# Kernel optimization log

Measured on AMD Instinct MI355X. Metric: run time of the kernel, lower is better.

Reference implementation:

```python
import jax, jax.numpy as jnp
import numpy as np

SOS = 28          # RNNTParam.SOS = num_labels - 1
NUM_EMBED = 28    # num_labels - 1
C = 320           # pred_hidden_size
L = 2             # pred_num_layers
U, N = 128, 512   # decode steps, batch


def setup_inputs() -> dict:
    key = jax.random.key(0)
    ks = jax.random.split(key, 8)
    s = 1.0 / np.sqrt(C).astype(np.float32)
    x = jax.random.randint(ks[0], (U, N), 0, 29)                       # labels incl. SOS=28
    h0 = jax.random.normal(ks[1], (L, N, C), jnp.float32)
    c0 = jax.random.normal(ks[2], (L, N, C), jnp.float32)
    embed_weight = jax.random.normal(ks[3], (NUM_EMBED, C), jnp.float32)
    w_ih = jax.random.uniform(ks[4], (L, 4 * C, C), jnp.float32, -s, s)
    w_hh = jax.random.uniform(ks[5], (L, 4 * C, C), jnp.float32, -s, s)
    b_ih = jax.random.uniform(ks[6], (L, 4 * C), jnp.float32, -s, s)
    b_hh = jax.random.uniform(ks[7], (L, 4 * C), jnp.float32, -s, s)
    return dict(x=x, h0=h0, c0=c0, embed_weight=embed_weight,
                w_ih=w_ih, w_hh=w_hh, b_ih=b_ih, b_hh=b_hh)


def _lstm_layer(xs, h0, c0, w_ih, w_hh, b_ih, b_hh):
    # xs: [U, N, C]; torch LSTM gate order: i, f, g, o
    bias = b_ih + b_hh                                   # [4C]
    gx = jnp.einsum('unc,gc->ung', xs, w_ih) + bias      # precompute input part

    def step(carry, gx_t):
        h, c = carry
        gates = gx_t + h @ w_hh.T                        # [N, 4C]
        i, f, g, o = jnp.split(gates, 4, axis=-1)
        i = jax.nn.sigmoid(i)
        f = jax.nn.sigmoid(f)
        g = jnp.tanh(g)
        o = jax.nn.sigmoid(o)
        c = f * c + i * g
        h = o * jnp.tanh(c)
        return (h, c), h

    (hT, cT), ys = jax.lax.scan(step, (h0, c0), gx)
    return ys, hT, cT


def reference(x, h0, c0, embed_weight, w_ih, w_hh, b_ih, b_hh):
    sos_mask = (x == SOS)                                # [U, N]
    idx = jnp.where(sos_mask, 0, x)
    g = embed_weight[idx]                                # [U, N, C]
    g = jnp.where(sos_mask[..., None], 0.0, g)

    hs, cs = [], []
    for layer in range(L):
        g, hT, cT = _lstm_layer(g, h0[layer], c0[layer],
                                w_ih[layer], w_hh[layer],
                                b_ih[layer], b_hh[layer])
        hs.append(hT)
        cs.append(cT)
    hg = jnp.stack(hs, axis=0)                           # [L, N, C]
    cg = jnp.stack(cs, axis=0)
    return g, (hg, cg)
```

## Files before the change

kernel.cpp:

```cpp
#include <hip/hip_runtime.h>
#include <hip/hip_bf16.h>
#include <stdint.h>


typedef short short8 __attribute__((ext_vector_type(8)));
typedef float f32x4 __attribute__((ext_vector_type(4)));

#define USTEPS 128
#define HSZ    (512*320)
#define GSTEP  (512*320)
#define HGOFF  (128*512*320)
#define CGOFF  (HGOFF + 2*512*320)
#define FLAGSTRIDE 16

__device__ __forceinline__ uint16_t f2bf(float f) {
  union { float f; uint32_t i; } v; v.f = f;
  uint32_t i = v.i;
  return (uint16_t)((i + 0x7fffu + ((i >> 16) & 1u)) >> 16);
}
__device__ __forceinline__ float rcp_(float x) { return __builtin_amdgcn_rcpf(x); }
__device__ __forceinline__ float sigm(float x) { return rcp_(1.0f + __expf(-x)); }
__device__ __forceinline__ float tanh_(float x) {
  float ax = fabsf(x);
  float e  = __expf(-2.0f * ax);
  float t  = (1.0f - e) * rcp_(1.0f + e);
  return x < 0.0f ? -t : t;
}
__device__ __forceinline__ uint4 cvt8(const float* s) {
  float4 a = ((const float4*)s)[0];
  float4 b = ((const float4*)s)[1];
  uint4 r;
  r.x = (uint32_t)f2bf(a.x) | ((uint32_t)f2bf(a.y) << 16);
  r.y = (uint32_t)f2bf(a.z) | ((uint32_t)f2bf(a.w) << 16);
  r.z = (uint32_t)f2bf(b.x) | ((uint32_t)f2bf(b.y) << 16);
  r.w = (uint32_t)f2bf(b.z) | ((uint32_t)f2bf(b.w) << 16);
  return r;
}
__device__ __forceinline__ short8 loadw8(const float* p) {
  float4 a = ((const float4*)p)[0];
  float4 b = ((const float4*)p)[1];
  short8 r;
  r[0] = (short)f2bf(a.x); r[1] = (short)f2bf(a.y);
  r[2] = (short)f2bf(a.z); r[3] = (short)f2bf(a.w);
  r[4] = (short)f2bf(b.x); r[5] = (short)f2bf(b.y);
  r[6] = (short)f2bf(b.z); r[7] = (short)f2bf(b.w);
  return r;
}

#define PREP_G0   (29 * 1280)
#define PREP_B1   (PREP_G0 + 1280)
#define PREP_FL   (PREP_B1 + 4096)
#define PREP_HI   (PREP_FL + 2 * 512 * 40)
__global__ void prep_kernel(const float* __restrict__ embed,
                            const float* __restrict__ w_ih,
                            const float* __restrict__ b_ih,
                            const float* __restrict__ b_hh,
                            const float* __restrict__ h0,
                            float* __restrict__ G0p,
                            float* __restrict__ bias1p,
                            uint32_t* __restrict__ flags,
                            uint16_t* __restrict__ Hx0,
                            uint16_t* __restrict__ Hx1) {
  int tid = blockIdx.x * blockDim.x + threadIdx.x;
  if (tid < PREP_G0) {
    int v = tid / 1280, col = tid % 1280;
    int hg = col / 80, idx = col % 80;
    int k = idx >> 2, q = idx & 3;
    int r = q * 320 + hg * 20 + k;
    float acc = b_ih[r] + b_hh[r];
    if (v < 28) {
      const float4* e = (const float4*)(embed + (size_t)v * 320);
      const float4* w = (const float4*)(w_ih + (size_t)r * 320);
#pragma unroll 4
      for (int i = 0; i < 80; ++i) {
        float4 a = e[i], b = w[i];
        acc += a.x * b.x + a.y * b.y + a.z * b.z + a.w * b.w;
      }
    }
    G0p[tid] = acc;
  } else if (tid < PREP_B1) {
    int col = tid - PREP_G0;
    int hg = col / 80, idx = col % 80;
    int k = idx >> 2, q = idx & 3;
    int r = q * 320 + hg * 20 + k;
    bias1p[col] = b_ih[1280 + r] + b_hh[1280 + r];
  } else if (tid < PREP_FL) {
    flags[tid - PREP_B1] = 0;
  } else if (tid < PREP_HI) {
    int id = tid - PREP_FL;
    int layer = id / 20480;
    int rem = id - layer * 20480;
    int n = rem / 40, c = rem - n * 40;
    const float* src = h0 + (size_t)layer * HSZ + (size_t)n * 320 + c * 8;
    uint16_t* dst = (layer ? Hx1 : Hx0) + HSZ + (size_t)n * 320 + c * 8;
    *(uint4*)dst = cvt8(src);
  }
}

__global__ void __launch_bounds__(320, 2)
rnnt_kernel(const int* __restrict__ x,
            const float* __restrict__ c0,
            const float* __restrict__ w_ih,
            const float* __restrict__ w_hh,
            const float* __restrict__ G0p,
            const float* __restrict__ bias1p,
            uint16_t* __restrict__ Hx0,
            uint16_t* __restrict__ Hx1,
            uint32_t* __restrict__ flags,
            float* __restrict__ out) {
  __shared__ __align__(16) uint16_t Hl0[32 * 320];
  __shared__ __align__(16) uint16_t Hl1[32 * 320];
  __shared__ __align__(16) float    gates0[32 * 84];
  __shared__ __align__(16) float    gates1[32 * 84];

  const int tid  = threadIdx.x;
  const int wave = tid >> 6;
  const int lane = tid & 63;
  const int quad = lane >> 4;
  const int lm   = lane & 15;
  const int blk  = blockIdx.x;
  const int bg = (blk & 7) * 2 + (blk >> 7);
  const int hg = (blk >> 3) & 15;

  short8 Bhh0[10], Bih1[10], Bhh1[10];
  {
    int ncol = wave * 16 + lm;
    int k = ncol >> 2, q = ncol & 3;
    int r = q * 320 + hg * 20 + k;
    const float* p0 = w_hh + (size_t)r * 320 + quad * 8;
    const float* p1 = w_hh + (size_t)(1280 + r) * 320 + quad * 8;
    const float* pi = w_ih + (size_t)(1280 + r) * 320 + quad * 8;
#pragma unroll
    for (int kk = 0; kk < 10; ++kk) {
      Bhh0[kk] = loadw8(p0 + kk * 32);
      Bhh1[kk] = loadw8(p1 + kk * 32);
      Bih1[kk] = loadw8(pi + kk * 32);
    }
  }
  const float bias1v = bias1p[hg * 80 + wave * 16 + lm];

  const int un  = tid / 10;
  const int ukp = tid - un * 10;
  const int n_g = bg * 32 + un;
  const int kc  = hg * 20 + ukp * 2;

  int smc[8], spc[8];
#pragma unroll
  for (int it = 0; it < 8; ++it) {
    int cid = tid + it * 320;
    int m = cid / 80;
    int c8 = cid - m * 80;
    int c16 = c8 >> 1, h = c8 & 1;
    int p16 = c16 + m; if (p16 >= 40) p16 -= 40;
    smc[it] = m * 320 + c8 * 4;
    spc[it] = m * 320 + p16 * 8 + h * 4;
  }
  const size_t gbase = (size_t)bg * 32 * 320;

  float c0s0 = c0[(size_t)n_g * 320 + kc];
  float c0s1 = c0[(size_t)n_g * 320 + kc + 1];
  float c1s0 = c0[(size_t)(512 + n_g) * 320 + kc];
  float c1s1 = c0[(size_t)(512 + n_g) * 320 + kc + 1];

  uint32_t* myflag = flags + (size_t)(bg * 16 + hg) * FLAGSTRIDE;

  float4 gxa, gxb;
  {
    const int v = x[n_g];
    const float* gx = G0p + (size_t)v * 1280 + hg * 80 + ukp * 8;
    gxa = ((const float4*)gx)[0];
    gxb = ((const float4*)gx)[1];
  }

#pragma unroll 1
  for (int t = 0; t <= USTEPS; ++t) {
    const bool do0 = (t < USTEPS);
    const bool do1 = (t >= 1);

    const uint16_t* s0b = Hx0 + (size_t)((t - 1) & 1) * HSZ + gbase;
    const uint16_t* s1b = Hx1 + (size_t)(t & 1) * HSZ + gbase;

    unsigned long long r0[8], r1[8];
#pragma unroll
    for (int it = 0; it < 8; ++it)
      r0[it] = __hip_atomic_load((unsigned long long*)(s0b + smc[it]),
                                 __ATOMIC_RELAXED, __HIP_MEMORY_SCOPE_AGENT);
#pragma unroll
    for (int it = 0; it < 8; ++it)
      r1[it] = __hip_atomic_load((unsigned long long*)(s1b + smc[it]),
                                 __ATOMIC_RELAXED, __HIP_MEMORY_SCOPE_AGENT);
#pragma unroll
    for (int it = 0; it < 8; ++it) {
      *(unsigned long long*)(Hl0 + spc[it]) = r0[it];
      *(unsigned long long*)(Hl1 + spc[it]) = r1[it];
    }
    __syncthreads();

    f32x4 ag00 = {0.f, 0.f, 0.f, 0.f}, ag01 = {0.f, 0.f, 0.f, 0.f};
    f32x4 ag10 = {bias1v, bias1v, bias1v, bias1v}, ag11 = ag10;
#pragma unroll
    for (int kk = 0; kk < 10; ++kk) {
      int cch = kk * 4 + quad;
      int p0a = cch + lm;      if (p0a >= 40) p0a -= 40;
      int p1a = cch + lm + 16; if (p1a >= 40) p1a -= 40;
      short8 a00 = *(const short8*)(Hl0 + lm * 320 + p0a * 8);
      short8 a01 = *(const short8*)(Hl0 + (lm + 16) * 320 + p1a * 8);
      if (do0) {
        ag00 = __builtin_amdgcn_mfma_f32_16x16x32_bf16(a00, Bhh0[kk], ag00, 0, 0, 0);
        ag01 = __builtin_amdgcn_mfma_f32_16x16x32_bf16(a01, Bhh0[kk], ag01, 0, 0, 0);
      }
      if (do1) {
        short8 a10 = *(const short8*)(Hl1 + lm * 320 + p0a * 8);
        short8 a11 = *(const short8*)(Hl1 + (lm + 16) * 320 + p1a * 8);
        ag10 = __builtin_amdgcn_mfma_f32_16x16x32_bf16(a00, Bih1[kk], ag10, 0, 0, 0);
        ag11 = __builtin_amdgcn_mfma_f32_16x16x32_bf16(a01, Bih1[kk], ag11, 0, 0, 0);
        ag10 = __builtin_amdgcn_mfma_f32_16x16x32_bf16(a10, Bhh1[kk], ag10, 0, 0, 0);
        ag11 = __builtin_amdgcn_mfma_f32_16x16x32_bf16(a11, Bhh1[kk], ag11, 0, 0, 0);
      }
    }

    if (do0) {
#pragma unroll
      for (int r = 0; r < 4; ++r) {
        gates0[(quad * 4 + r) * 84 + wave * 16 + lm]      = ag00[r];
        gates0[(16 + quad * 4 + r) * 84 + wave * 16 + lm] = ag01[r];
      }
    }
    if (do1) {
#pragma unroll
      for (int r = 0; r < 4; ++r) {
        gates1[(quad * 4 + r) * 84 + wave * 16 + lm]      = ag10[r];
        gates1[(16 + quad * 4 + r) * 84 + wave * 16 + lm] = ag11[r];
      }
    }
    __syncthreads();

    if (do0) {
      const float* gp = gates0 + un * 84 + ukp * 8;
      float i0 = gp[0] + gxa.x, f0 = gp[1] + gxa.y, g0 = gp[2] + gxa.z, o0 = gp[3] + gxa.w;
      float i1 = gp[4] + gxb.x, f1 = gp[5] + gxb.y, g1 = gp[6] + gxb.z, o1 = gp[7] + gxb.w;
      c0s0 = sigm(f0) * c0s0 + sigm(i0) * tanh_(g0);
      c0s1 = sigm(f1) * c0s1 + sigm(i1) * tanh_(g1);
      float ha = sigm(o0) * tanh_(c0s0);
      float hb = sigm(o1) * tanh_(c0s1);
      uint32_t packed = (uint32_t)f2bf(ha) | ((uint32_t)f2bf(hb) << 16);
      __hip_atomic_store((uint32_t*)(Hx0 + (size_t)(t & 1) * HSZ + (size_t)n_g * 320 + kc),
                         packed, __ATOMIC_RELAXED, __HIP_MEMORY_SCOPE_AGENT);
      if (t == USTEPS - 1) {
        *(float2*)(out + HGOFF + (size_t)n_g * 320 + kc) = make_float2(ha, hb);
        *(float2*)(out + CGOFF + (size_t)n_g * 320 + kc) = make_float2(c0s0, c0s1);
      }
    }

    if (do1) {
      const int u1 = t - 1;
      const float* gp = gates1 + un * 84 + ukp * 8;
      float i0 = gp[0], f0 = gp[1], g0 = gp[2], o0 = gp[3];
      float i1 = gp[4], f1 = gp[5], g1 = gp[6], o1 = gp[7];
      c1s0 = sigm(f0) * c1s0 + sigm(i0) * tanh_(g0);
      c1s1 = sigm(f1) * c1s1 + sigm(i1) * tanh_(g1);
      float ha = sigm(o0) * tanh_(c1s0);
      float hb = sigm(o1) * tanh_(c1s1);
      *(float2*)(out + (size_t)u1 * GSTEP + (size_t)n_g * 320 + kc) = make_float2(ha, hb);
      uint32_t packed = (uint32_t)f2bf(ha) | ((uint32_t)f2bf(hb) << 16);
      __hip_atomic_store((uint32_t*)(Hx1 + (size_t)((t + 1) & 1) * HSZ + (size_t)n_g * 320 + kc),
                         packed, __ATOMIC_RELAXED, __HIP_MEMORY_SCOPE_AGENT);
      if (t == USTEPS) {
        *(float2*)(out + HGOFF + (size_t)(512 + n_g) * 320 + kc) = make_float2(ha, hb);
        *(float2*)(out + CGOFF + (size_t)(512 + n_g) * 320 + kc) = make_float2(c1s0, c1s1);
      }
    }

    if (t + 1 < USTEPS) {
      const int v = x[(t + 1) * 512 + n_g];
      const float* gx = G0p + (size_t)v * 1280 + hg * 80 + ukp * 8;
      gxa = ((const float4*)gx)[0];
      gxb = ((const float4*)gx)[1];
    }

    if (t < USTEPS) {
      asm volatile("s_waitcnt vmcnt(0)" ::: "memory");
      __syncthreads();
      if (tid < 16) {
        if (tid == 0) {
          __hip_atomic_store(myflag, (uint32_t)(t + 1), __ATOMIC_RELAXED,
                             __HIP_MEMORY_SCOPE_AGENT);
        }
        uint32_t* peer = flags + (size_t)(bg * 16 + tid) * FLAGSTRIDE;
        while (__hip_atomic_load(peer, __ATOMIC_RELAXED,
                                 __HIP_MEMORY_SCOPE_AGENT) < (uint32_t)(t + 1)) {
        }
      }
      __syncthreads();
    }
  }
}

extern "C" void kernel_launch(void* const* d_in, const int* in_sizes, int n_in,
                              void* d_out, int out_size, void* d_ws, size_t ws_size,
                              hipStream_t stream) {
  (void)in_sizes; (void)n_in; (void)out_size; (void)ws_size;
  const int*   x     = (const int*)d_in[0];
  const float* h0    = (const float*)d_in[1];
  const float* c0    = (const float*)d_in[2];
  const float* embed = (const float*)d_in[3];
  const float* w_ih  = (const float*)d_in[4];
  const float* w_hh  = (const float*)d_in[5];
  const float* b_ih  = (const float*)d_in[6];
  const float* b_hh  = (const float*)d_in[7];
  float* out = (float*)d_out;

  char* ws = (char*)d_ws;
  float*    G0p   = (float*)(ws);
  float*    b1p   = (float*)(ws + 148480);
  uint32_t* flags = (uint32_t*)(ws + 153600);
  uint16_t* Hx0   = (uint16_t*)(ws + 169984);
  uint16_t* Hx1   = (uint16_t*)(ws + 825344);

  hipLaunchKernelGGL(prep_kernel, dim3(326), dim3(256), 0, stream,
                     embed, w_ih, b_ih, b_hh, h0, G0p, b1p, flags, Hx0, Hx1);

  void* args[] = { (void*)&x, (void*)&c0, (void*)&w_ih, (void*)&w_hh,
                   (void*)&G0p, (void*)&b1p, (void*)&Hx0, (void*)&Hx1,
                   (void*)&flags, (void*)&out };
  hipLaunchCooperativeKernel((const void*)rnnt_kernel, dim3(256), dim3(320),
                             args, 0, stream);
}
```

Baseline: 748.1 us.

## Split grid barrier into per-layer flags and overlap layer-1 loads with compute

```diff
diff --git a/kernel.cpp b/kernel.cpp
--- a/kernel.cpp
+++ b/kernel.cpp
@@ -49,7 +49,7 @@
 
 #define PREP_G0   (29 * 1280)
 #define PREP_B1   (PREP_G0 + 1280)
-#define PREP_FL   (PREP_B1 + 4096)
+#define PREP_FL   (PREP_B1 + 8192)
 #define PREP_HI   (PREP_FL + 2 * 512 * 40)
 __global__ void prep_kernel(const float* __restrict__ embed,
                             const float* __restrict__ w_ih,
@@ -112,6 +112,7 @@
   __shared__ __align__(16) uint16_t Hl1[32 * 320];
   __shared__ __align__(16) float    gates0[32 * 84];
   __shared__ __align__(16) float    gates1[32 * 84];
+  __shared__ int ctr0, ctr1;
 
   const int tid  = threadIdx.x;
   const int wave = tid >> 6;
@@ -162,7 +163,25 @@
   float c1s0 = c0[(size_t)(512 + n_g) * 320 + kc];
   float c1s1 = c0[(size_t)(512 + n_g) * 320 + kc + 1];
 
-  uint32_t* myflag = flags + (size_t)(bg * 16 + hg) * FLAGSTRIDE;
+  uint32_t* flags0  = flags;
+  uint32_t* flags1  = flags + 256 * FLAGSTRIDE;
+  uint32_t* myflag0 = flags0 + (size_t)(bg * 16 + hg) * FLAGSTRIDE;
+  uint32_t* myflag1 = flags1 + (size_t)(bg * 16 + hg) * FLAGSTRIDE;
+
+  {
+    if (tid == 0) { ctr0 = 0; ctr1 = 0; }
+    const uint16_t* s0b = Hx0 + HSZ + gbase;
+    unsigned long long r0[8];
+#pragma unroll
+    for (int it = 0; it < 8; ++it)
+      r0[it] = __hip_atomic_load((const unsigned long long*)(s0b + smc[it]),
+                                 __ATOMIC_RELAXED, __HIP_MEMORY_SCOPE_AGENT);
+    asm volatile("s_waitcnt vmcnt(0)" ::: "memory");
+#pragma unroll
+    for (int it = 0; it < 8; ++it)
+      *(unsigned long long*)(Hl0 + spc[it]) = r0[it];
+    __syncthreads();
+  }
 
   float4 gxa, gxb;
   {
@@ -177,24 +196,14 @@
     const bool do0 = (t < USTEPS);
     const bool do1 = (t >= 1);
 
-    const uint16_t* s0b = Hx0 + (size_t)((t - 1) & 1) * HSZ + gbase;
-    const uint16_t* s1b = Hx1 + (size_t)(t & 1) * HSZ + gbase;
-
-    unsigned long long r0[8], r1[8];
-#pragma unroll
-    for (int it = 0; it < 8; ++it)
-      r0[it] = __hip_atomic_load((unsigned long long*)(s0b + smc[it]),
-                                 __ATOMIC_RELAXED, __HIP_MEMORY_SCOPE_AGENT);
-#pragma unroll
-    for (int it = 0; it < 8; ++it)
-      r1[it] = __hip_atomic_load((unsigned long long*)(s1b + smc[it]),
-                                 __ATOMIC_RELAXED, __HIP_MEMORY_SCOPE_AGENT);
-#pragma unroll
-    for (int it = 0; it < 8; ++it) {
-      *(unsigned long long*)(Hl0 + spc[it]) = r0[it];
-      *(unsigned long long*)(Hl1 + spc[it]) = r1[it];
-    }
-    __syncthreads();
+    unsigned long long r1[8];
+    if (do1) {
+      const uint16_t* s1b = Hx1 + (size_t)(t & 1) * HSZ + gbase;
+#pragma unroll
+      for (int it = 0; it < 8; ++it)
+        r1[it] = __hip_atomic_load((const unsigned long long*)(s1b + smc[it]),
+                                   __ATOMIC_RELAXED, __HIP_MEMORY_SCOPE_AGENT);
+    }
 
     f32x4 ag00 = {0.f, 0.f, 0.f, 0.f}, ag01 = {0.f, 0.f, 0.f, 0.f};
     f32x4 ag10 = {bias1v, bias1v, bias1v, bias1v}, ag11 = ag10;
@@ -210,27 +219,22 @@
         ag01 = __builtin_amdgcn_mfma_f32_16x16x32_bf16(a01, Bhh0[kk], ag01, 0, 0, 0);
       }
       if (do1) {
-        short8 a10 = *(const short8*)(Hl1 + lm * 320 + p0a * 8);
-        short8 a11 = *(const short8*)(Hl1 + (lm + 16) * 320 + p1a * 8);
         ag10 = __builtin_amdgcn_mfma_f32_16x16x32_bf16(a00, Bih1[kk], ag10, 0, 0, 0);
         ag11 = __builtin_amdgcn_mfma_f32_16x16x32_bf16(a01, Bih1[kk], ag11, 0, 0, 0);
-        ag10 = __builtin_amdgcn_mfma_f32_16x16x32_bf16(a10, Bhh1[kk], ag10, 0, 0, 0);
-        ag11 = __builtin_amdgcn_mfma_f32_16x16x32_bf16(a11, Bhh1[kk], ag11, 0, 0, 0);
-      }
-    }
-
+      }
+    }
+
+    if (do1) {
+      asm volatile("s_waitcnt vmcnt(0)" ::: "memory");
+#pragma unroll
+      for (int it = 0; it < 8; ++it)
+        *(unsigned long long*)(Hl1 + spc[it]) = r1[it];
+    }
     if (do0) {
 #pragma unroll
       for (int r = 0; r < 4; ++r) {
         gates0[(quad * 4 + r) * 84 + wave * 16 + lm]      = ag00[r];
         gates0[(16 + quad * 4 + r) * 84 + wave * 16 + lm] = ag01[r];
-      }
-    }
-    if (do1) {
-#pragma unroll
-      for (int r = 0; r < 4; ++r) {
-        gates1[(quad * 4 + r) * 84 + wave * 16 + lm]      = ag10[r];
-        gates1[(16 + quad * 4 + r) * 84 + wave * 16 + lm] = ag11[r];
       }
     }
     __syncthreads();
@@ -251,6 +255,48 @@
         *(float2*)(out + CGOFF + (size_t)n_g * 320 + kc) = make_float2(c0s0, c0s1);
       }
     }
+
+    if (do1) {
+#pragma unroll
+      for (int kk = 0; kk < 5; ++kk) {
+        int cch = kk * 4 + quad;
+        int p0a = cch + lm;      if (p0a >= 40) p0a -= 40;
+        int p1a = cch + lm + 16; if (p1a >= 40) p1a -= 40;
+        short8 a10 = *(const short8*)(Hl1 + lm * 320 + p0a * 8);
+        short8 a11 = *(const short8*)(Hl1 + (lm + 16) * 320 + p1a * 8);
+        ag10 = __builtin_amdgcn_mfma_f32_16x16x32_bf16(a10, Bhh1[kk], ag10, 0, 0, 0);
+        ag11 = __builtin_amdgcn_mfma_f32_16x16x32_bf16(a11, Bhh1[kk], ag11, 0, 0, 0);
+      }
+    }
+
+    if (do0) {
+      asm volatile("s_waitcnt vmcnt(0)" ::: "memory");
+      if (lane == 0) {
+        int old = atomicAdd(&ctr0, 1);
+        if ((old % 5) == 4)
+          __hip_atomic_store(myflag0, (uint32_t)(t + 1), __ATOMIC_RELAXED,
+                             __HIP_MEMORY_SCOPE_AGENT);
+      }
+    }
+
+    if (do1) {
+#pragma unroll
+      for (int kk = 5; kk < 10; ++kk) {
+        int cch = kk * 4 + quad;
+        int p0a = cch + lm;      if (p0a >= 40) p0a -= 40;
+        int p1a = cch + lm + 16; if (p1a >= 40) p1a -= 40;
+        short8 a10 = *(const short8*)(Hl1 + lm * 320 + p0a * 8);
+        short8 a11 = *(const short8*)(Hl1 + (lm + 16) * 320 + p1a * 8);
+        ag10 = __builtin_amdgcn_mfma_f32_16x16x32_bf16(a10, Bhh1[kk], ag10, 0, 0, 0);
+        ag11 = __builtin_amdgcn_mfma_f32_16x16x32_bf16(a11, Bhh1[kk], ag11, 0, 0, 0);
+      }
+#pragma unroll
+      for (int r = 0; r < 4; ++r) {
+        gates1[(quad * 4 + r) * 84 + wave * 16 + lm]      = ag10[r];
+        gates1[(16 + quad * 4 + r) * 84 + wave * 16 + lm] = ag11[r];
+      }
+    }
+    __syncthreads();
 
     if (do1) {
       const int u1 = t - 1;
@@ -269,6 +315,13 @@
         *(float2*)(out + HGOFF + (size_t)(512 + n_g) * 320 + kc) = make_float2(ha, hb);
         *(float2*)(out + CGOFF + (size_t)(512 + n_g) * 320 + kc) = make_float2(c1s0, c1s1);
       }
+      asm volatile("s_waitcnt vmcnt(0)" ::: "memory");
+      if (lane == 0) {
+        int old = atomicAdd(&ctr1, 1);
+        if ((old % 5) == 4)
+          __hip_atomic_store(myflag1, (uint32_t)(t + 1), __ATOMIC_RELAXED,
+                             __HIP_MEMORY_SCOPE_AGENT);
+      }
     }
 
     if (t + 1 < USTEPS) {
@@ -279,14 +332,25 @@
     }
 
     if (t < USTEPS) {
+      if (tid < 16) {
+        uint32_t* peer = flags0 + (size_t)(bg * 16 + tid) * FLAGSTRIDE;
+        while (__hip_atomic_load(peer, __ATOMIC_RELAXED,
+                                 __HIP_MEMORY_SCOPE_AGENT) < (uint32_t)(t + 1)) {
+        }
+      }
+      __syncthreads();
+      const uint16_t* s0b = Hx0 + (size_t)(t & 1) * HSZ + gbase;
+      unsigned long long r0[8];
+#pragma unroll
+      for (int it = 0; it < 8; ++it)
+        r0[it] = __hip_atomic_load((const unsigned long long*)(s0b + smc[it]),
+                                   __ATOMIC_RELAXED, __HIP_MEMORY_SCOPE_AGENT);
       asm volatile("s_waitcnt vmcnt(0)" ::: "memory");
-      __syncthreads();
-      if (tid < 16) {
-        if (tid == 0) {
-          __hip_atomic_store(myflag, (uint32_t)(t + 1), __ATOMIC_RELAXED,
-                             __HIP_MEMORY_SCOPE_AGENT);
-        }
-        uint32_t* peer = flags + (size_t)(bg * 16 + tid) * FLAGSTRIDE;
+#pragma unroll
+      for (int it = 0; it < 8; ++it)
+        *(unsigned long long*)(Hl0 + spc[it]) = r0[it];
+      if (tid < 16 && t >= 1) {
+        uint32_t* peer = flags1 + (size_t)(bg * 16 + tid) * FLAGSTRIDE;
         while (__hip_atomic_load(peer, __ATOMIC_RELAXED,
                                  __HIP_MEMORY_SCOPE_AGENT) < (uint32_t)(t + 1)) {
         }
@@ -314,10 +378,10 @@
   float*    G0p   = (float*)(ws);
   float*    b1p   = (float*)(ws + 148480);
   uint32_t* flags = (uint32_t*)(ws + 153600);
-  uint16_t* Hx0   = (uint16_t*)(ws + 169984);
-  uint16_t* Hx1   = (uint16_t*)(ws + 825344);
-
-  hipLaunchKernelGGL(prep_kernel, dim3(326), dim3(256), 0, stream,
+  uint16_t* Hx0   = (uint16_t*)(ws + 186368);
+  uint16_t* Hx1   = (uint16_t*)(ws + 841728);
+
+  hipLaunchKernelGGL(prep_kernel, dim3(342), dim3(256), 0, stream,
                      embed, w_ih, b_ih, b_hh, h0, G0p, b1p, flags, Hx0, Hx1);
 
   void* args[] = { (void*)&x, (void*)&c0, (void*)&w_ih, (void*)&w_hh,
```

New measurement: 757.5 us. Within noise of the previous version (+1.3%).
